# Kernel tuning notes

Measured on AMD Instinct MI355X. Metric: run time of the kernel, lower is better.

The kernel has to match this reference:

```python
import jax, jax.numpy as jnp
import numpy as np

N, E = 50000, 800000
NODE_DIM, EDGE_DIM, HEADS = 64, 16, 4
C = NODE_DIM // HEADS  # per-head channels
NEG_SLOPE = 0.2
BN_EPS = 1e-5


def setup_inputs() -> dict:
    key = jax.random.key(0)
    ks = jax.random.split(key, 12)
    glorot = lambda k, shape: jax.random.normal(k, shape, jnp.float32) * np.sqrt(2.0 / (shape[0] + shape[-1]))
    return {
        "x": jax.random.normal(ks[0], (N, NODE_DIM), jnp.float32),
        "edge_index": jax.random.randint(ks[1], (2, E), 0, N, jnp.int32),
        "edge_attr": jax.random.normal(ks[2], (E, EDGE_DIM), jnp.float32),
        "W_l": glorot(ks[3], (NODE_DIM, HEADS * C)),
        "b_l": jnp.zeros((HEADS * C,), jnp.float32),
        "W_r": glorot(ks[4], (NODE_DIM, HEADS * C)),
        "b_r": jnp.zeros((HEADS * C,), jnp.float32),
        "W_e": glorot(ks[5], (EDGE_DIM, HEADS * C)),
        "att": glorot(ks[6], (HEADS, C)),
        "bias": jnp.zeros((HEADS * C,), jnp.float32),
        "gamma": jnp.ones((NODE_DIM,), jnp.float32),
        "beta": jnp.zeros((NODE_DIM,), jnp.float32),
    }


def reference(x, edge_index, edge_attr, W_l, b_l, W_r, b_r, W_e, att, bias, gamma, beta):
    src, dst = edge_index[0], edge_index[1]
    n = x.shape[0]
    # GATv2: node transforms for source (l) and target (r) roles
    xl = (x @ W_l + b_l).reshape(n, HEADS, C)
    xr = (x @ W_r + b_r).reshape(n, HEADS, C)
    e = (edge_attr @ W_e).reshape(-1, HEADS, C)
    # per-edge attention logits: leaky_relu(x_j + x_i + e) . att  -> [E, H]
    g = jax.nn.leaky_relu(xl[src] + xr[dst] + e, NEG_SLOPE)
    logits = jnp.einsum('ehc,hc->eh', g, att)
    # segment softmax grouped by destination node
    amax = jax.ops.segment_max(logits, dst, num_segments=n)
    ex = jnp.exp(logits - amax[dst])
    denom = jax.ops.segment_sum(ex, dst, num_segments=n)
    alpha = ex / (denom[dst] + 1e-16)  # [E, H]
    # weighted message aggregation (scatter-add over dst), concat heads
    msg = xl[src] * alpha[..., None]  # [E, H, C]
    out = jax.ops.segment_sum(msg, dst, num_segments=n).reshape(n, HEADS * C) + bias
    # BatchNorm (training-mode batch statistics over nodes)
    mean = out.mean(axis=0)
    var = out.var(axis=0)
    out = (out - mean) * jax.lax.rsqrt(var + BN_EPS) * gamma + beta
    # residual + exact GELU
    return jax.nn.gelu(out + x, approximate=False)
```

## Files before the change

### kernel.cpp

```cpp
#include <hip/hip_runtime.h>
#include <hip/hip_fp16.h>
#include <math.h>

#define NODE_DIM 64
#define EDGE_DIM 16
#define CAP 64
#define NEG_SLOPE 0.2f
#define BN_EPS 1e-5f

typedef unsigned short ushort_t;
typedef unsigned int uint_t;
typedef __fp16 h2_t __attribute__((ext_vector_type(2)));

template<int CTRL>
__device__ __forceinline__ float dpp_mov_f(float v) {
    return __int_as_float(__builtin_amdgcn_update_dpp(
        0, __float_as_int(v), CTRL, 0xF, 0xF, true));
}
__device__ __forceinline__ float row_sum16(float v) {
    v += dpp_mov_f<0x128>(v);
    v += dpp_mov_f<0x124>(v);
    v += dpp_mov_f<0x122>(v);
    v += dpp_mov_f<0x121>(v);
    return v;
}
__device__ __forceinline__ float wave_sum64(float v) {
    v = row_sum16(v);
    v += __shfl_xor(v, 16, 64);
    v += __shfl_xor(v, 32, 64);
    return v;
}
__device__ __forceinline__ float wave_max64(float v) {
    v = fmaxf(v, dpp_mov_f<0x128>(v));
    v = fmaxf(v, dpp_mov_f<0x124>(v));
    v = fmaxf(v, dpp_mov_f<0x122>(v));
    v = fmaxf(v, dpp_mov_f<0x121>(v));
    v = fmaxf(v, __shfl_xor(v, 16, 64));
    v = fmaxf(v, __shfl_xor(v, 32, 64));
    return v;
}
__device__ __forceinline__ ushort_t f2bf(float f) {
    unsigned int b = __float_as_uint(f);
    b += 0x7FFFu + ((b >> 16) & 1u);
    return (ushort_t)(b >> 16);
}
__device__ __forceinline__ float bf2f(ushort_t u) {
    return __uint_as_float(((unsigned int)u) << 16);
}
__device__ __forceinline__ uint_t packh2(float a, float b) {
    __half2 h;
    h.x = __float2half_rn(a);
    h.y = __float2half_rn(b);
    return *reinterpret_cast<uint_t*>(&h);
}
__device__ __forceinline__ float2 unpackh2(uint_t u) {
    __half2 h = *reinterpret_cast<__half2*>(&u);
    return make_float2(__half2float(h.x), __half2float(h.y));
}
__device__ __forceinline__ float fdot2u(uint_t a, uint_t b, float c) {
#if __has_builtin(__builtin_amdgcn_fdot2)
    union { uint_t u; h2_t h; } ua, ub;
    ua.u = a; ub.u = b;
    return __builtin_amdgcn_fdot2(ua.h, ub.h, c, false);
#else
    float2 fa = unpackh2(a), fb = unpackh2(b);
    return fmaf(fa.y, fb.y, fmaf(fa.x, fb.x, c));
#endif
}

__global__ __launch_bounds__(256) void k_transform(
    const float* __restrict__ x, const float* __restrict__ Wl,
    const float* __restrict__ bl, const float* __restrict__ Wr,
    const float* __restrict__ br, ushort_t* __restrict__ xlbf,
    ushort_t* __restrict__ xrbf, int n)
{
    int lane = threadIdx.x & 63;
    int wid = threadIdx.x >> 6;

    uint_t wlp[32], wrp[32];
#pragma unroll
    for (int m = 0; m < 32; m++) {
        wlp[m] = packh2(Wl[(2 * m) * NODE_DIM + lane],
                        Wl[(2 * m + 1) * NODE_DIM + lane]);
        wrp[m] = packh2(Wr[(2 * m) * NODE_DIM + lane],
                        Wr[(2 * m + 1) * NODE_DIM + lane]);
    }
    float blc = bl[lane], brc = br[lane];

    for (int row = blockIdx.x * 4 + wid; row < n; row += gridDim.x * 4) {
        const float4* x4 = (const float4*)(x + (size_t)row * NODE_DIM);
        float al = blc, ar = brc;
#pragma unroll
        for (int p = 0; p < 16; p++) {
            float4 v = x4[p];
            uint_t x01 = packh2(v.x, v.y);
            uint_t x23 = packh2(v.z, v.w);
            al = fdot2u(x01, wlp[2 * p], al);
            al = fdot2u(x23, wlp[2 * p + 1], al);
            ar = fdot2u(x01, wrp[2 * p], ar);
            ar = fdot2u(x23, wrp[2 * p + 1], ar);
        }
        xlbf[(size_t)row * NODE_DIM + lane] = f2bf(al);
        xrbf[(size_t)row * NODE_DIM + lane] = f2bf(ar);
    }
}

__global__ __launch_bounds__(256) void k_edge(
    const int* __restrict__ ei, const float* __restrict__ eattr,
    const float* __restrict__ We, const float* __restrict__ att,
    int* __restrict__ cursors,
    const ushort_t* __restrict__ xlbf, const ushort_t* __restrict__ xrbf,
    int* __restrict__ slots, uint4* __restrict__ payload, int E)
{
    __shared__ uint_t sea[4][64 * 8];
    __shared__ float slg[4][64 * 4];

    int lane = threadIdx.x & 63;
    int wid = threadIdx.x >> 6;
    int wbase = (blockIdx.x * 4 + wid) * 64;
    if (wbase >= E) return;
    wbase = __builtin_amdgcn_readfirstlane(wbase);
    int cnt = E - wbase; if (cnt > 64) cnt = 64;

    {
        const float4* esrc = (const float4*)(eattr + (size_t)wbase * EDGE_DIM);
        uint2* sdst = (uint2*)sea[wid];
        int lim = cnt * 4;
#pragma unroll
        for (int r = 0; r < 4; r++) {
            int idx = r * 64 + lane;
            if (idx < lim) {
                float4 v = esrc[idx];
                sdst[idx] = make_uint2(packh2(v.x, v.y), packh2(v.z, v.w));
            }
        }
    }

    uint_t wep[8];
#pragma unroll
    for (int m = 0; m < 8; m++)
        wep[m] = packh2(We[(2 * m) * NODE_DIM + lane],
                        We[(2 * m + 1) * NODE_DIM + lane]);
    float att_p = att[lane];
    float att_n = att_p * NEG_SLOPE;

    int src_l = 0;
    if (lane < cnt) {
        src_l = ei[wbase + lane];
        int dst_l = ei[E + wbase + lane];
        int pos_l = atomicAdd(&cursors[dst_l], 1);
        if (pos_l < CAP) slots[(size_t)dst_l * CAP + pos_l] = wbase + lane;
    }
    int dst_l_bc = (lane < cnt) ? ei[E + wbase + lane] : 0;

    uint_t* seaW = sea[wid];
    float* slgW = slg[wid];

    ushort_t pxl[8], pxr[8];
    auto LOADT = [&](int t, int k) {
        int s = __builtin_amdgcn_readlane(src_l, t);
        int d = __builtin_amdgcn_readlane(dst_l_bc, t);
        pxl[k] = xlbf[(size_t)s * NODE_DIM + lane];
        pxr[k] = xrbf[(size_t)d * NODE_DIM + lane];
    };
    auto COMP = [&](int t, int k) {
        const uint4* e4 = (const uint4*)(seaW + t * 8);
        uint4 ea0 = e4[0], ea1 = e4[1];
        float p0 = 0.f, p1 = 0.f;
        p0 = fdot2u(ea0.x, wep[0], p0);  p1 = fdot2u(ea0.y, wep[1], p1);
        p0 = fdot2u(ea0.z, wep[2], p0);  p1 = fdot2u(ea0.w, wep[3], p1);
        p0 = fdot2u(ea1.x, wep[4], p0);  p1 = fdot2u(ea1.y, wep[5], p1);
        p0 = fdot2u(ea1.z, wep[6], p0);  p1 = fdot2u(ea1.w, wep[7], p1);
        float sv = bf2f(pxl[k]) + bf2f(pxr[k]) + (p0 + p1);
        float g = sv * (sv > 0.f ? att_p : att_n);
        g = row_sum16(g);
        if ((lane & 15) == 0) slgW[t * 4 + (lane >> 4)] = g;
    };

    if (cnt == 64) {
#pragma unroll
        for (int k = 0; k < 8; k++) LOADT(k, k);
#pragma unroll 1
        for (int tb = 0; tb < 56; tb += 8) {
#pragma unroll
            for (int k = 0; k < 8; k++) {
                COMP(tb + k, k);
                LOADT(tb + k + 8, k);
            }
        }
#pragma unroll
        for (int k = 0; k < 8; k++) COMP(56 + k, k);
    } else {
#pragma unroll
        for (int k = 0; k < 8; k++) if (k < cnt) LOADT(k, k);
        for (int tb = 0; tb < cnt; tb += 8) {
#pragma unroll
            for (int k = 0; k < 8; k++) {
                int t = tb + k;
                if (t < cnt) {
                    COMP(t, k);
                    int tn = t + 8;
                    if (tn < cnt) LOADT(tn, k);
                }
            }
        }
    }

    if (lane < cnt) {
        float4 lg4 = ((const float4*)slgW)[lane];
        payload[wbase + lane] =
            make_uint4((uint_t)src_l, packh2(lg4.x, lg4.y),
                       packh2(lg4.z, lg4.w), 0u);
    }
}

__global__ __launch_bounds__(256) void k_fused(
    const int* __restrict__ slots, const uint4* __restrict__ payload,
    const int* __restrict__ cursors, const ushort_t* __restrict__ xlbf,
    const float* __restrict__ bias, float* __restrict__ out, int n)
{
    __shared__ float salpha[4][CAP * 4];
    __shared__ int ssrc[4][CAP];

    int wid = threadIdx.x >> 6;
    int lane = threadIdx.x & 63;
    int i = blockIdx.x * 4 + wid;
    if (i >= n) return;

    int deg = cursors[i];
    if (deg > CAP) deg = CAP;
    bool act = (lane < deg);

    int eid = act ? slots[(size_t)i * CAP + lane] : 0;
    uint4 pl = act ? payload[eid] : make_uint4(0u, 0u, 0u, 0u);
    int se_x = (int)pl.x;
    float2 g01 = unpackh2(pl.y);
    float2 g23 = unpackh2(pl.z);

    float l0 = act ? g01.x : -1e30f;
    float l1 = act ? g01.y : -1e30f;
    float l2 = act ? g23.x : -1e30f;
    float l3 = act ? g23.y : -1e30f;
    float m0 = wave_max64(l0), m1 = wave_max64(l1);
    float m2 = wave_max64(l2), m3 = wave_max64(l3);
    float e0 = act ? __expf(l0 - m0) : 0.f;
    float e1 = act ? __expf(l1 - m1) : 0.f;
    float e2 = act ? __expf(l2 - m2) : 0.f;
    float e3 = act ? __expf(l3 - m3) : 0.f;
    float s0 = wave_sum64(e0), s1 = wave_sum64(e1);
    float s2 = wave_sum64(e2), s3 = wave_sum64(e3);
    float* salW = salpha[wid];
    int* ssrcW = ssrc[wid];
    ((float4*)salW)[lane] = make_float4(
        e0 / (s0 + 1e-16f), e1 / (s1 + 1e-16f),
        e2 / (s2 + 1e-16f), e3 / (s3 + 1e-16f));
    ssrcW[lane] = se_x;

    int r = lane >> 3, c = lane & 7;
    float a0 = 0.f, a1 = 0.f, a2 = 0.f, a3 = 0.f;
    float a4 = 0.f, a5 = 0.f, a6 = 0.f, a7 = 0.f;
    int nb = (deg + 7) >> 3;
    for (int b = 0; b < nb; b++) {
        int t = b * 8 + r;
        int src_t = ssrcW[t];
        float al = salW[t * 4 + (c >> 1)];
        uint4 v = *(const uint4*)(xlbf + (size_t)src_t * NODE_DIM + c * 8);
        a0 = fmaf(al, __uint_as_float(v.x << 16), a0);
        a1 = fmaf(al, __uint_as_float(v.x & 0xFFFF0000u), a1);
        a2 = fmaf(al, __uint_as_float(v.y << 16), a2);
        a3 = fmaf(al, __uint_as_float(v.y & 0xFFFF0000u), a3);
        a4 = fmaf(al, __uint_as_float(v.z << 16), a4);
        a5 = fmaf(al, __uint_as_float(v.z & 0xFFFF0000u), a5);
        a6 = fmaf(al, __uint_as_float(v.w << 16), a6);
        a7 = fmaf(al, __uint_as_float(v.w & 0xFFFF0000u), a7);
    }
#define RED(x) do { \
        x += dpp_mov_f<0x128>(x); \
        x += __shfl_xor(x, 16, 64); \
        x += __shfl_xor(x, 32, 64); } while (0)
    RED(a0); RED(a1); RED(a2); RED(a3);
    RED(a4); RED(a5); RED(a6); RED(a7);
#undef RED
    float t0 = (r & 1) ? a1 : a0;
    float t1 = (r & 1) ? a3 : a2;
    float t2 = (r & 1) ? a5 : a4;
    float t3 = (r & 1) ? a7 : a6;
    float u0 = (r & 2) ? t1 : t0;
    float u1 = (r & 2) ? t3 : t2;
    float w  = (r & 4) ? u1 : u0;
    int ch = c * 8 + r;
    out[(size_t)i * NODE_DIM + ch] = w + bias[ch];
}

__global__ __launch_bounds__(256) void k_bnstat(
    const float* __restrict__ out, float* __restrict__ stats, int n)
{
    __shared__ float sbuf[256];
    int col = threadIdx.x & 63;
    int rgrp = threadIdx.x >> 6;
    float s = 0.f, q = 0.f;
    for (int row = blockIdx.x * 4 + rgrp; row < n; row += gridDim.x * 4) {
        float v = out[(size_t)row * 64 + col];
        s += v;
        q = fmaf(v, v, q);
    }
    sbuf[threadIdx.x] = s;
    __syncthreads();
    if (threadIdx.x < 64) {
        s = sbuf[threadIdx.x] + sbuf[threadIdx.x + 64] +
            sbuf[threadIdx.x + 128] + sbuf[threadIdx.x + 192];
        atomicAdd(&stats[col], s);
    }
    __syncthreads();
    sbuf[threadIdx.x] = q;
    __syncthreads();
    if (threadIdx.x < 64) {
        q = sbuf[threadIdx.x] + sbuf[threadIdx.x + 64] +
            sbuf[threadIdx.x + 128] + sbuf[threadIdx.x + 192];
        atomicAdd(&stats[64 + col], q);
    }
}

__global__ __launch_bounds__(256) void k_final(
    float* __restrict__ out, const float* __restrict__ x,
    const float* __restrict__ stats, const float* __restrict__ gamma,
    const float* __restrict__ beta, int total, float invn)
{
    int i = blockIdx.x * 256 + threadIdx.x;
    if (i >= total) return;
    int c = i & 63;
    float mean = stats[c] * invn;
    float var = stats[64 + c] * invn - mean * mean;
    float z = (out[i] - mean) * rsqrtf(var + BN_EPS) * gamma[c] + beta[c] + x[i];
    out[i] = z * 0.5f * (1.f + erff(z * 0.70710678118654752f));
}

extern "C" void kernel_launch(void* const* d_in, const int* in_sizes, int n_in,
                              void* d_out, int out_size, void* d_ws, size_t ws_size,
                              hipStream_t stream)
{
    const float* x     = (const float*)d_in[0];
    const int*   ei    = (const int*)d_in[1];
    const float* eattr = (const float*)d_in[2];
    const float* Wl    = (const float*)d_in[3];
    const float* bl    = (const float*)d_in[4];
    const float* Wr    = (const float*)d_in[5];
    const float* br    = (const float*)d_in[6];
    const float* We    = (const float*)d_in[7];
    const float* att   = (const float*)d_in[8];
    const float* bias  = (const float*)d_in[9];
    const float* gamma = (const float*)d_in[10];
    const float* beta  = (const float*)d_in[11];
    int n = in_sizes[0] / NODE_DIM;
    int E = in_sizes[1] / 2;

    char* ws = (char*)d_ws;
    ushort_t* xlbf    = (ushort_t*)ws; ws += (size_t)n * NODE_DIM * 2;
    ushort_t* xrbf    = (ushort_t*)ws; ws += (size_t)n * NODE_DIM * 2;
    uint4*    payload = (uint4*)ws;    ws += (size_t)E * 16;
    int*      slots   = (int*)ws;      ws += (size_t)n * CAP * 4;
    int*      cursors = (int*)ws;      ws += (size_t)n * 4;
    float*    stats   = (float*)ws;    ws += 128 * 4;

    hipMemsetAsync(cursors, 0, (size_t)(n + 128) * 4, stream);

    k_transform<<<1024, 256, 0, stream>>>(x, Wl, bl, Wr, br, xlbf, xrbf, n);
    k_edge<<<(E + 255) / 256, 256, 0, stream>>>(
        ei, eattr, We, att, cursors, xlbf, xrbf, slots, payload, E);
    k_fused<<<(n + 3) / 4, 256, 0, stream>>>(
        slots, payload, cursors, xlbf, bias, (float*)d_out, n);
    k_bnstat<<<256, 256, 0, stream>>>((const float*)d_out, stats, n);
    k_final<<<(n * NODE_DIM + 255) / 256, 256, 0, stream>>>(
        (float*)d_out, x, stats, gamma, beta, n * NODE_DIM, 1.0f / n);
}
```

Baseline: 175.6 us.

## Scatter edge payloads directly into per-node slots and batch gather loads

k_edge now writes each edge's packed payload (src plus half-precision logits) straight into the destination node's bucket at the atomically reserved position. This removes the separate slots index array and the dependent indirect load in k_fused, where payload is now read contiguously. The aggregation loop is also fully unrolled so that up to eight neighbour rows are loaded before any accumulation, raising memory-level parallelism. In exchange, payload storage grows to n*CAP uint4 entries, the scattered 16-byte writes are random, and register pressure rises.

Result: faster. 165.3 us (-5.9%).

```diff
diff --git a/kernel.cpp b/kernel.cpp
--- a/kernel.cpp
+++ b/kernel.cpp
@@ -110,7 +110,7 @@
     const float* __restrict__ We, const float* __restrict__ att,
     int* __restrict__ cursors,
     const ushort_t* __restrict__ xlbf, const ushort_t* __restrict__ xrbf,
-    int* __restrict__ slots, uint4* __restrict__ payload, int E)
+    uint4* __restrict__ payload, int E)
 {
     __shared__ uint_t sea[4][64 * 8];
     __shared__ float slg[4][64 * 4];
@@ -144,14 +144,13 @@
     float att_p = att[lane];
     float att_n = att_p * NEG_SLOPE;
 
-    int src_l = 0;
+    int src_l = 0, pos_l = CAP, dst_l = 0;
     if (lane < cnt) {
         src_l = ei[wbase + lane];
-        int dst_l = ei[E + wbase + lane];
-        int pos_l = atomicAdd(&cursors[dst_l], 1);
-        if (pos_l < CAP) slots[(size_t)dst_l * CAP + pos_l] = wbase + lane;
-    }
-    int dst_l_bc = (lane < cnt) ? ei[E + wbase + lane] : 0;
+        dst_l = ei[E + wbase + lane];
+        pos_l = atomicAdd(&cursors[dst_l], 1);
+    }
+    int dst_l_bc = dst_l;
 
     uint_t* seaW = sea[wid];
     float* slgW = slg[wid];
@@ -206,18 +205,18 @@
         }
     }
 
-    if (lane < cnt) {
+    if (lane < cnt && pos_l < CAP) {
         float4 lg4 = ((const float4*)slgW)[lane];
-        payload[wbase + lane] =
+        payload[(size_t)dst_l * CAP + pos_l] =
             make_uint4((uint_t)src_l, packh2(lg4.x, lg4.y),
                        packh2(lg4.z, lg4.w), 0u);
     }
 }
 
 __global__ __launch_bounds__(256) void k_fused(
-    const int* __restrict__ slots, const uint4* __restrict__ payload,
-    const int* __restrict__ cursors, const ushort_t* __restrict__ xlbf,
-    const float* __restrict__ bias, float* __restrict__ out, int n)
+    const uint4* __restrict__ payload, const int* __restrict__ cursors,
+    const ushort_t* __restrict__ xlbf, const float* __restrict__ bias,
+    float* __restrict__ out, int n)
 {
     __shared__ float salpha[4][CAP * 4];
     __shared__ int ssrc[4][CAP];
@@ -231,8 +230,7 @@
     if (deg > CAP) deg = CAP;
     bool act = (lane < deg);
 
-    int eid = act ? slots[(size_t)i * CAP + lane] : 0;
-    uint4 pl = act ? payload[eid] : make_uint4(0u, 0u, 0u, 0u);
+    uint4 pl = act ? payload[(size_t)i * CAP + lane] : make_uint4(0u, 0u, 0u, 0u);
     int se_x = (int)pl.x;
     float2 g01 = unpackh2(pl.y);
     float2 g23 = unpackh2(pl.z);
@@ -260,20 +258,33 @@
     float a0 = 0.f, a1 = 0.f, a2 = 0.f, a3 = 0.f;
     float a4 = 0.f, a5 = 0.f, a6 = 0.f, a7 = 0.f;
     int nb = (deg + 7) >> 3;
-    for (int b = 0; b < nb; b++) {
-        int t = b * 8 + r;
-        int src_t = ssrcW[t];
-        float al = salW[t * 4 + (c >> 1)];
-        uint4 v = *(const uint4*)(xlbf + (size_t)src_t * NODE_DIM + c * 8);
-        a0 = fmaf(al, __uint_as_float(v.x << 16), a0);
-        a1 = fmaf(al, __uint_as_float(v.x & 0xFFFF0000u), a1);
-        a2 = fmaf(al, __uint_as_float(v.y << 16), a2);
-        a3 = fmaf(al, __uint_as_float(v.y & 0xFFFF0000u), a3);
-        a4 = fmaf(al, __uint_as_float(v.z << 16), a4);
-        a5 = fmaf(al, __uint_as_float(v.z & 0xFFFF0000u), a5);
-        a6 = fmaf(al, __uint_as_float(v.w << 16), a6);
-        a7 = fmaf(al, __uint_as_float(v.w & 0xFFFF0000u), a7);
-    }
+
+    uint4 v0, v1, v2, v3, v4, v5, v6, v7;
+#define LDV(B, V)                                                        \
+    if ((B) < nb) {                                                      \
+        int st = ssrcW[(B) * 8 + r];                                     \
+        V = *(const uint4*)(xlbf + (size_t)st * NODE_DIM + c * 8);       \
+    }
+    LDV(0, v0) LDV(1, v1) LDV(2, v2) LDV(3, v3)
+    LDV(4, v4) LDV(5, v5) LDV(6, v6) LDV(7, v7)
+#undef LDV
+
+#define ACC(B, V)                                                        \
+    if ((B) < nb) {                                                      \
+        float al = salW[((B) * 8 + r) * 4 + (c >> 1)];                   \
+        a0 = fmaf(al, __uint_as_float(V.x << 16), a0);                   \
+        a1 = fmaf(al, __uint_as_float(V.x & 0xFFFF0000u), a1);           \
+        a2 = fmaf(al, __uint_as_float(V.y << 16), a2);                   \
+        a3 = fmaf(al, __uint_as_float(V.y & 0xFFFF0000u), a3);           \
+        a4 = fmaf(al, __uint_as_float(V.z << 16), a4);                   \
+        a5 = fmaf(al, __uint_as_float(V.z & 0xFFFF0000u), a5);           \
+        a6 = fmaf(al, __uint_as_float(V.w << 16), a6);                   \
+        a7 = fmaf(al, __uint_as_float(V.w & 0xFFFF0000u), a7);           \
+    }
+    ACC(0, v0) ACC(1, v1) ACC(2, v2) ACC(3, v3)
+    ACC(4, v4) ACC(5, v5) ACC(6, v6) ACC(7, v7)
+#undef ACC
+
 #define RED(x) do { \
         x += dpp_mov_f<0x128>(x); \
         x += __shfl_xor(x, 16, 64); \
@@ -357,8 +368,7 @@
     char* ws = (char*)d_ws;
     ushort_t* xlbf    = (ushort_t*)ws; ws += (size_t)n * NODE_DIM * 2;
     ushort_t* xrbf    = (ushort_t*)ws; ws += (size_t)n * NODE_DIM * 2;
-    uint4*    payload = (uint4*)ws;    ws += (size_t)E * 16;
-    int*      slots   = (int*)ws;      ws += (size_t)n * CAP * 4;
+    uint4*    payload = (uint4*)ws;    ws += (size_t)n * CAP * 16;
     int*      cursors = (int*)ws;      ws += (size_t)n * 4;
     float*    stats   = (float*)ws;    ws += 128 * 4;
 
@@ -366,9 +376,9 @@
 
     k_transform<<<1024, 256, 0, stream>>>(x, Wl, bl, Wr, br, xlbf, xrbf, n);
     k_edge<<<(E + 255) / 256, 256, 0, stream>>>(
-        ei, eattr, We, att, cursors, xlbf, xrbf, slots, payload, E);
+        ei, eattr, We, att, cursors, xlbf, xrbf, payload, E);
     k_fused<<<(n + 3) / 4, 256, 0, stream>>>(
-        slots, payload, cursors, xlbf, bias, (float*)d_out, n);
+        payload, cursors, xlbf, bias, (float*)d_out, n);
     k_bnstat<<<256, 256, 0, stream>>>((const float*)d_out, stats, n);
     k_final<<<(n * NODE_DIM + 255) / 256, 256, 0, stream>>>(
         (float*)d_out, x, stats, gamma, beta, n * NODE_DIM, 1.0f / n);
```
